# Performance work log

Hardware: AMD Instinct MI355X
Metric: run time of the kernel (lower is better)

The kernel has to match this reference:

```python
import jax, jax.numpy as jnp
import numpy as np

D_MODEL = 1024
N_HEADS = 16
HDIM = D_MODEL // N_HEADS
IMP_EPS = 1e-6


def setup_inputs() -> dict:
    key = jax.random.key(0)
    ks = jax.random.split(key, 7)
    B, T_q, T_kv, N_s = 2, 2048, 256, 16
    scale = 1.0 / np.sqrt(D_MODEL)
    return {
        "query": jax.random.normal(ks[0], (B, T_q, D_MODEL), dtype=jnp.float32),
        "key_value": jax.random.normal(ks[1], (B, T_kv, N_s, D_MODEL), dtype=jnp.float32),
        "imp_weights": jax.random.uniform(ks[2], (B, N_s), dtype=jnp.float32),
        "W_q": jax.random.normal(ks[3], (D_MODEL, D_MODEL), dtype=jnp.float32) * scale,
        "W_k": jax.random.normal(ks[4], (D_MODEL, D_MODEL), dtype=jnp.float32) * scale,
        "W_v": jax.random.normal(ks[5], (D_MODEL, D_MODEL), dtype=jnp.float32) * scale,
        "W_o": jax.random.normal(ks[6], (D_MODEL, D_MODEL), dtype=jnp.float32) * scale,
    }


def _split_heads(x):
    # [B, T, D] -> [B, h, T, d]
    B, T, _ = x.shape
    return x.reshape(B, T, N_HEADS, HDIM).transpose(0, 2, 1, 3)


def reference(query, key_value, imp_weights, W_q, W_k, W_v, W_o):
    # CAU_MultiheadCrossAttention.forward with 4D key_value (sensor axis).
    B, T_q, D = query.shape
    _, T_kv, N_s, _ = key_value.shape
    kv = key_value.reshape(B, T_kv * N_s, D)  # flatten sensor axis into source length S

    qh = _split_heads(query @ W_q.T)   # [B,h,T_q,d]  (nn.Linear: x @ W.T)
    kh = _split_heads(kv @ W_k.T)      # [B,h,S,d]
    vh = _split_heads(kv @ W_v.T)      # [B,h,S,d]

    # importance: [B,N_s] -> tiled over T_kv -> [B, S], log-clamped additive mask
    imp_full = jnp.broadcast_to(imp_weights[:, None, :], (B, T_kv, N_s)).reshape(B, T_kv * N_s)
    log_imp = jnp.log(jnp.clip(imp_full, IMP_EPS, None)).astype(qh.dtype)  # [B,S]

    scores = jnp.einsum("bhqd,bhkd->bhqk", qh, kh) / np.sqrt(HDIM).astype(np.float32)
    scores = scores + log_imp[:, None, None, :]
    attn = jax.nn.softmax(scores, axis=-1)
    y = jnp.einsum("bhqk,bhkd->bhqd", attn, vh)  # [B,h,T_q,d]

    y = y.transpose(0, 2, 1, 3).reshape(B, T_q, D)  # merge heads
    return y @ W_o.T
```

## Files before the change

kernel.cpp:

```cpp
#include <hip/hip_runtime.h>
#include <hip/hip_bf16.h>

typedef __bf16    bf16x8_t __attribute__((ext_vector_type(8)));
typedef __bf16    bf16x4_t __attribute__((ext_vector_type(4)));
typedef float     f32x4_t  __attribute__((ext_vector_type(4)));
typedef float     f32x16_t __attribute__((ext_vector_type(16)));
typedef _Float16  f16x8_t  __attribute__((ext_vector_type(8)));
typedef unsigned int u32x2_t __attribute__((ext_vector_type(2)));
typedef unsigned int u32x4_t __attribute__((ext_vector_type(4)));

static __device__ __forceinline__ f32x4_t mfma16(bf16x8_t a, bf16x8_t b, f32x4_t c) {
    return __builtin_amdgcn_mfma_f32_16x16x32_bf16(a, b, c, 0, 0, 0);
}
static __device__ __forceinline__ f32x16_t mfma32(bf16x8_t a, bf16x8_t b, f32x16_t c) {
    return __builtin_amdgcn_mfma_f32_32x32x16_bf16(a, b, c, 0, 0, 0);
}
static __device__ __forceinline__ f32x16_t zero16() {
    f32x16_t z;
#pragma unroll
    for (int j = 0; j < 16; j++) z[j] = 0.f;
    return z;
}

static __device__ __forceinline__ void async16(const __bf16* g, __bf16* l) {
    __builtin_amdgcn_global_load_lds(
        (const __attribute__((address_space(1))) unsigned int*)g,
        (__attribute__((address_space(3))) unsigned int*)l, 16, 0, 0);
}

__global__ __launch_bounds__(256) void f2b_multi(const float* __restrict__ q,
                                                 const float* __restrict__ kv,
                                                 const float* __restrict__ wq,
                                                 const float* __restrict__ wk,
                                                 const float* __restrict__ wv,
                                                 const float* __restrict__ wo,
                                                 __bf16* __restrict__ qb,
                                                 __bf16* __restrict__ kvb,
                                                 __bf16* __restrict__ wqb,
                                                 __bf16* __restrict__ wkvb,
                                                 __bf16* __restrict__ wob,
                                                 float qscale) {
    int i = blockIdx.x * 256 + threadIdx.x;
    const float* src; __bf16* dst; int base; float scale = 1.0f;
    if (i < 1048576)      { src = q;  dst = qb;   base = 0; }
    else if (i < 3145728) { src = kv; dst = kvb;  base = 1048576; }
    else if (i < 3407872) { src = wq; dst = wqb;  base = 3145728; scale = qscale; }
    else if (i < 3670016) { src = wk; dst = wkvb; base = 3407872; }
    else if (i < 3932160) { src = wv; dst = wkvb + 1048576; base = 3670016; }
    else                  { src = wo; dst = wob;  base = 3932160; }
    int j = i - base;
    float4 v = reinterpret_cast<const float4*>(src)[j];
    bf16x4_t o;
    o[0] = (__bf16)(v.x * scale); o[1] = (__bf16)(v.y * scale);
    o[2] = (__bf16)(v.z * scale); o[3] = (__bf16)(v.w * scale);
    reinterpret_cast<bf16x4_t*>(dst)[j] = o;
}

__global__ __launch_bounds__(256) void proj_kernel(const __bf16* __restrict__ qb,
                                                   const __bf16* __restrict__ wqb,
                                                   const __bf16* __restrict__ kvb,
                                                   const __bf16* __restrict__ wkvb,
                                                   __bf16* __restrict__ Qp,
                                                   __bf16* __restrict__ Khd,
                                                   __bf16* __restrict__ Vhd,
                                                   const float* __restrict__ imp) {
    __shared__ __bf16 As[128 * 32];
    __shared__ __bf16 Bs[128 * 32];
    __shared__ __bf16 Es[2][4096];

    const int gid = blockIdx.x;
    const __bf16 *A, *B;
    long m0, n0;
    int mode;
    if (gid < 256) {
        m0 = (long)(gid >> 3) * 128; n0 = (long)(gid & 7) * 128;
        A = qb; B = wqb; mode = 0;
    } else {
        int g2 = gid - 256;
        m0 = (long)(g2 >> 4) * 128; n0 = (long)(g2 & 15) * 128;
        A = kvb; B = wkvb; mode = (n0 < 1024) ? 1 : 2;
    }

    const int t    = threadIdx.x;
    const int w    = t >> 6;
    const int lane = t & 63;
    const int quad = lane >> 4;
    const int mn   = lane & 15;
    const int wm   = (w & 1) * 64;
    const int wn   = (w >> 1) * 64;

    const int  srow = t >> 2;
    const int  scol = (t & 3) * 8;
    const __bf16* gA = A + (m0 + srow) * 1024 + scol;
    const __bf16* gB = B + (n0 + srow) * 1024 + scol;

    f32x4_t acc[4][4];
#pragma unroll
    for (int i = 0; i < 4; i++)
#pragma unroll
        for (int j = 0; j < 4; j++) acc[i][j] = (f32x4_t){0.f, 0.f, 0.f, 0.f};

    for (int k0 = 0; k0 < 1024; k0 += 32) {
        __syncthreads();
        async16(gA + k0,              &As[t * 8]);
        async16(gA + 64 * 1024 + k0,  &As[2048 + t * 8]);
        async16(gB + k0,              &Bs[t * 8]);
        async16(gB + 64 * 1024 + k0,  &Bs[2048 + t * 8]);
        __syncthreads();

        bf16x8_t af[4], bf[4];
#pragma unroll
        for (int i = 0; i < 4; i++)
            af[i] = *(const bf16x8_t*)&As[(wm + i * 16 + mn) * 32 + quad * 8];
#pragma unroll
        for (int j = 0; j < 4; j++)
            bf[j] = *(const bf16x8_t*)&Bs[(wn + j * 16 + mn) * 32 + quad * 8];
#pragma unroll
        for (int i = 0; i < 4; i++)
#pragma unroll
            for (int j = 0; j < 4; j++) acc[i][j] = mfma16(af[i], bf[j], acc[i][j]);
    }

    __syncthreads();
    __bf16* stg = (w == 0) ? As : (w == 1) ? Bs : Es[w - 2];

    if (mode != 2) {
#pragma unroll
        for (int i = 0; i < 4; i++)
#pragma unroll
            for (int j = 0; j < 4; j++)
#pragma unroll
                for (int r = 0; r < 4; r++) {
                    int sl = i * 16 + quad * 4 + r;
                    int d  = j * 16 + mn;
                    stg[sl * 64 + (((d >> 3) ^ (sl & 7)) * 8) + (d & 7)] =
                        (__bf16)acc[i][j][r];
                }
    } else {
        const int b_ = (int)((m0 + wm) >> 12);
        float scl[4];
#pragma unroll
        for (int r = 0; r < 4; r++)
            scl[r] = fmaxf(imp[b_ * 16 + quad * 4 + r], 1e-6f);
#pragma unroll
        for (int i = 0; i < 4; i++)
#pragma unroll
            for (int j = 0; j < 4; j++) {
                bf16x4_t pk;
#pragma unroll
                for (int r = 0; r < 4; r++) pk[r] = (__bf16)(acc[i][j][r] * scl[r]);
                int d  = j * 16 + mn;
                int s0 = i * 16 + quad * 4;
                *(bf16x4_t*)&stg[d * 64 + (((s0 >> 3) ^ (d & 7)) * 8) + (s0 & 7)] = pk;
            }
    }

    if (mode == 0) {
        __bf16* Cg = Qp + (m0 + wm) * 1024 + (n0 + wn);
#pragma unroll
        for (int it = 0; it < 8; it++) {
            int rowL = it * 8 + (lane >> 3);
            int cb   = lane & 7;
            bf16x8_t vv = *(const bf16x8_t*)&stg[rowL * 64 + ((cb ^ (rowL & 7)) * 8)];
            *(bf16x8_t*)&Cg[(long)rowL * 1024 + cb * 8] = vv;
        }
    } else {
        const int b_    = (int)((m0 + wm) >> 12);
        const int sbase = (int)((m0 + wm) & 4095);
        __bf16* dst;
        if (mode == 1) {
            int h_ = (int)((n0 + wn) >> 6);
            dst = Khd + (long)(b_ * 16 + h_) * 262144 + (long)sbase * 64;
        } else {
            int h_ = (int)((n0 + wn) >> 6) - 16;
            dst = Vhd + (long)(b_ * 16 + h_) * 262144 + (long)(sbase >> 6) * 4096;
        }
#pragma unroll
        for (int it = 0; it < 8; it++) {
            int rowL = it * 8 + (lane >> 3);
            int cb   = lane & 7;
            bf16x8_t vv = *(const bf16x8_t*)&stg[rowL * 64 + ((cb ^ (rowL & 7)) * 8)];
            *(bf16x8_t*)&dst[rowL * 64 + cb * 8] = vv;
        }
    }
}

__global__ __launch_bounds__(256, 4) void attn_kernel(const __bf16* __restrict__ Qp,
                                                      const __bf16* __restrict__ Kh,
                                                      const __bf16* __restrict__ Vh,
                                                      const float* __restrict__ imp,
                                                      _Float16* __restrict__ Op,
                                                      float* __restrict__ Lp) {
    const int gid = blockIdx.x;
    const int qt  = (gid >> 3) & 15;
    const int sp  = (gid >> 7) & 1;
    const int bh  = ((gid >> 8) << 3) | (gid & 7);
    const int b   = bh >> 4;
    const int h   = bh & 15;
    const int t    = threadIdx.x;
    const int w    = t >> 6;
    const int lane = t & 63;
    const int hi   = lane >> 5;
    const int q32  = lane & 31;

    __shared__ __bf16 Ks[2][64 * 64];
    __shared__ __bf16 Vs[64 * 64];

    const long qrow0 = (long)b * 2048 + qt * 128 + w * 32;
    const __bf16* Kb = Kh + (long)bh * 262144;
    const __bf16* Vb = Vh + (long)bh * 262144;

    const int r8 = lane >> 3;
    const int cs = (lane & 7) ^ r8;
    const int soff    = r8 * 64 + cs * 8;
    const int srcoff0 = (0 * 4 + w) * 512 + soff;
    const int srcoff1 = (1 * 4 + w) * 512 + soff;

    bf16x8_t aq[4];
#pragma unroll
    for (int ks = 0; ks < 4; ks++)
        aq[ks] = *(const bf16x8_t*)&Qp[(qrow0 + q32) * 1024 + h * 64 + ks * 16 + hi * 8];

    float lp[2][4];
#pragma unroll
    for (int j = 0; j < 2; j++)
#pragma unroll
        for (int r = 0; r < 4; r++) lp[j][r] = 0.f;
    f32x16_t o0 = zero16(), o1 = zero16();

    const int st0 = sp * 32;

    async16(Kb + (long)st0 * 4096 + srcoff0, &Ks[0][(0 * 4 + w) * 512]);
    async16(Kb + (long)st0 * 4096 + srcoff1, &Ks[0][(1 * 4 + w) * 512]);

    const int sw8 = q32 & 7;

    for (int it = 0; it < 32; ++it) {
        const int st  = st0 + it;
        const int cur = it & 1;

        __syncthreads();

        async16(Vb + (long)st * 4096 + srcoff0, &Vs[(0 * 4 + w) * 512]);
        async16(Vb + (long)st * 4096 + srcoff1, &Vs[(1 * 4 + w) * 512]);

        const __bf16* Kc = &Ks[cur][0];
        bf16x8_t pa[4];

#pragma unroll
        for (int st2 = 0; st2 < 2; st2++) {
            f32x16_t sc = zero16();
            __builtin_amdgcn_s_setprio(1);
#pragma unroll
            for (int ks = 0; ks < 4; ks++) {
                bf16x8_t kf = *(const bf16x8_t*)
                    &Kc[(st2 * 32 + q32) * 64 + ((((ks << 1) | hi) ^ sw8) << 3)];
                sc = mfma32(kf, aq[ks], sc);
            }
            __builtin_amdgcn_s_setprio(0);

            unsigned int wv[8];
#pragma unroll
            for (int g = 0; g < 4; g++) {
                float p0 = __builtin_amdgcn_exp2f(sc[4 * g + 0]);
                float p1 = __builtin_amdgcn_exp2f(sc[4 * g + 1]);
                float p2 = __builtin_amdgcn_exp2f(sc[4 * g + 2]);
                float p3 = __builtin_amdgcn_exp2f(sc[4 * g + 3]);
                lp[g & 1][0] += p0; lp[g & 1][1] += p1;
                lp[g & 1][2] += p2; lp[g & 1][3] += p3;
                bf16x4_t pk;
                pk[0] = (__bf16)p0; pk[1] = (__bf16)p1;
                pk[2] = (__bf16)p2; pk[3] = (__bf16)p3;
                u32x2_t uu = __builtin_bit_cast(u32x2_t, pk);
                wv[2 * g]     = uu[0];
                wv[2 * g + 1] = uu[1];
            }
            u32x2_t s02 = __builtin_amdgcn_permlane32_swap(wv[0], wv[2], false, false);
            u32x2_t s13 = __builtin_amdgcn_permlane32_swap(wv[1], wv[3], false, false);
            u32x2_t s46 = __builtin_amdgcn_permlane32_swap(wv[4], wv[6], false, false);
            u32x2_t s57 = __builtin_amdgcn_permlane32_swap(wv[5], wv[7], false, false);
            u32x4_t pu0 = {s02[0], s13[0], s02[1], s13[1]};
            u32x4_t pu1 = {s46[0], s57[0], s46[1], s57[1]};
            pa[st2 * 2 + 0] = __builtin_bit_cast(bf16x8_t, pu0);
            pa[st2 * 2 + 1] = __builtin_bit_cast(bf16x8_t, pu1);
        }

        __syncthreads();

        async16(Kb + (long)(st + 1) * 4096 + srcoff0, &Ks[cur ^ 1][(0 * 4 + w) * 512]);
        async16(Kb + (long)(st + 1) * 4096 + srcoff1, &Ks[cur ^ 1][(1 * 4 + w) * 512]);

        __builtin_amdgcn_s_setprio(1);
#pragma unroll
        for (int ks = 0; ks < 4; ks++) {
            bf16x8_t v0 = *(const bf16x8_t*)
                &Vs[(0 * 32 + q32) * 64 + ((((ks << 1) | hi) ^ sw8) << 3)];
            bf16x8_t v1 = *(const bf16x8_t*)
                &Vs[(1 * 32 + q32) * 64 + ((((ks << 1) | hi) ^ sw8) << 3)];
            o0 = mfma32(pa[ks], v0, o0);
            o1 = mfma32(pa[ks], v1, o1);
        }
        __builtin_amdgcn_s_setprio(0);
    }

    float lsum = 0.f;
#pragma unroll
    for (int j = 0; j < 2; j++)
#pragma unroll
        for (int r = 0; r < 4; r++)
            lsum += lp[j][r] * fmaxf(imp[b * 16 + 4 * hi + 8 * j + r], 1e-6f);
    lsum += __shfl_xor(lsum, 32);
    if (lane < 32)
        Lp[((long)sp * 4096 + qrow0 + q32) * 16 + h] = lsum;

#pragma unroll
    for (int j = 0; j < 16; j++) {
        int q_loc = (j & 3) + 8 * (j >> 2) + 4 * hi;
        long row  = (long)sp * 4096 + qrow0 + q_loc;
        Op[row * 1024 + h * 64 + 0 * 32 + q32] = (_Float16)o0[j];
        Op[row * 1024 + h * 64 + 1 * 32 + q32] = (_Float16)o1[j];
    }
}

__global__ __launch_bounds__(256) void combine_kernel(const _Float16* __restrict__ Op,
                                                      const float* __restrict__ Lp,
                                                      __bf16* __restrict__ Y) {
    int tid = blockIdx.x * 256 + threadIdx.x;
    int row = tid >> 7;
    int cg  = tid & 127;
    int h   = cg >> 3;
    f16x8_t o0 = *(const f16x8_t*)&Op[(long)row * 1024 + cg * 8];
    f16x8_t o1 = *(const f16x8_t*)&Op[(long)(4096 + row) * 1024 + cg * 8];
    float inv = 1.0f / (Lp[row * 16 + h] + Lp[(4096 + row) * 16 + h]);
    bf16x8_t y;
#pragma unroll
    for (int j = 0; j < 8; j++) y[j] = (__bf16)(((float)o0[j] + (float)o1[j]) * inv);
    *(bf16x8_t*)&Y[(long)row * 1024 + cg * 8] = y;
}

__global__ __launch_bounds__(256) void gemm_out_kernel(const __bf16* __restrict__ A,
                                                       const __bf16* __restrict__ B,
                                                       float* __restrict__ P) {
    __shared__ __bf16 As[128 * 32];
    __shared__ __bf16 Bs[128 * 32];

    const int  kh = blockIdx.x >> 3;
    const long n0 = (long)(blockIdx.x & 7) * 128;
    const long m0 = (long)blockIdx.y * 128;
    const int  kb = kh * 512;
    float* C = P + (long)kh * 4194304;

    const int t    = threadIdx.x;
    const int w    = t >> 6;
    const int lane = t & 63;
    const int quad = lane >> 4;
    const int mn   = lane & 15;
    const int wm   = (w & 1) * 64;
    const int wn   = (w >> 1) * 64;

    const int  srow = t >> 2;
    const int  scol = (t & 3) * 8;
    const __bf16* gA = A + (m0 + srow) * 1024 + kb + scol;
    const __bf16* gB = B + (n0 + srow) * 1024 + kb + scol;

    f32x4_t acc[4][4];
#pragma unroll
    for (int i = 0; i < 4; i++)
#pragma unroll
        for (int j = 0; j < 4; j++) acc[i][j] = (f32x4_t){0.f, 0.f, 0.f, 0.f};

    for (int k0 = 0; k0 < 512; k0 += 32) {
        __syncthreads();
        async16(gA + k0,             &As[t * 8]);
        async16(gA + 64 * 1024 + k0, &As[2048 + t * 8]);
        async16(gB + k0,             &Bs[t * 8]);
        async16(gB + 64 * 1024 + k0, &Bs[2048 + t * 8]);
        __syncthreads();

        bf16x8_t af[4], bf[4];
#pragma unroll
        for (int i = 0; i < 4; i++)
            af[i] = *(const bf16x8_t*)&As[(wm + i * 16 + mn) * 32 + quad * 8];
#pragma unroll
        for (int j = 0; j < 4; j++)
            bf[j] = *(const bf16x8_t*)&Bs[(wn + j * 16 + mn) * 32 + quad * 8];
#pragma unroll
        for (int i = 0; i < 4; i++)
#pragma unroll
            for (int j = 0; j < 4; j++) acc[i][j] = mfma16(af[i], bf[j], acc[i][j]);
    }

#pragma unroll
    for (int i = 0; i < 4; i++)
#pragma unroll
        for (int j = 0; j < 4; j++)
#pragma unroll
            for (int r = 0; r < 4; r++) {
                long row = m0 + wm + i * 16 + quad * 4 + r;
                long col = n0 + wn + j * 16 + mn;
                C[row * 1024 + col] = acc[i][j][r];
            }
}

__global__ __launch_bounds__(256) void combine2_kernel(const float* __restrict__ P0,
                                                       const float* __restrict__ P1,
                                                       float* __restrict__ out) {
    int i = blockIdx.x * 256 + threadIdx.x;
    float4 a = reinterpret_cast<const float4*>(P0)[i];
    float4 b = reinterpret_cast<const float4*>(P1)[i];
    float4 c; c.x = a.x + b.x; c.y = a.y + b.y; c.z = a.z + b.z; c.w = a.w + b.w;
    reinterpret_cast<float4*>(out)[i] = c;
}

extern "C" void kernel_launch(void* const* d_in, const int* in_sizes, int n_in,
                              void* d_out, int out_size, void* d_ws, size_t ws_size,
                              hipStream_t stream) {
    const float* q_f  = (const float*)d_in[0];
    const float* kv_f = (const float*)d_in[1];
    const float* imp  = (const float*)d_in[2];
    const float* wq_f = (const float*)d_in[3];
    const float* wk_f = (const float*)d_in[4];
    const float* wv_f = (const float*)d_in[5];
    const float* wo_f = (const float*)d_in[6];

    char* ws = (char*)d_ws;
    const size_t MB = 1ull << 20;
    __bf16*   qb    = (__bf16*)(ws + 0);
    __bf16*   kvb   = (__bf16*)(ws + 8 * MB);
    __bf16*   wqb   = (__bf16*)(ws + 24 * MB);
    __bf16*   wkvb  = (__bf16*)(ws + 26 * MB);
    _Float16* Opart = (_Float16*)(ws + 0);
    float*    Lpart = (float*)(ws + 16 * MB);
    __bf16*   Yb    = (__bf16*)(ws + 17 * MB);
    __bf16*   wob   = (__bf16*)(ws + 30 * MB);
    __bf16*   Qp    = (__bf16*)(ws + 32 * MB);
    __bf16*   Khd   = (__bf16*)(ws + 40 * MB);
    __bf16*   Vhd   = (__bf16*)(ws + 56 * MB);
    float*    Gp    = (float*)(ws + 40 * MB);

    const float QSCALE = 0.125f * 1.4426950408889634f;

    f2b_multi<<<16384, 256, 0, stream>>>(q_f, kv_f, wq_f, wk_f, wv_f, wo_f,
                                         qb, kvb, wqb, wkvb, wob, QSCALE);

    proj_kernel<<<1280, 256, 0, stream>>>(qb, wqb, kvb, wkvb, Qp, Khd, Vhd, imp);

    attn_kernel<<<1024, 256, 0, stream>>>(Qp, Khd, Vhd, imp, Opart, Lpart);
    combine_kernel<<<2048, 256, 0, stream>>>(Opart, Lpart, Yb);

    gemm_out_kernel<<<dim3(16, 32), 256, 0, stream>>>(Yb, wob, Gp);
    combine2_kernel<<<4096, 256, 0, stream>>>(Gp, Gp + 4194304, (float*)d_out);
}
```

Baseline: 292.1 us.

## Store K/V tiles in fragment-major layout to drop LDS swizzle addressing

The projection epilogue now writes K and V head tiles in the order the MFMA fragments consume them (8-element chunks grouped by k-slice), not row-major with an XOR swizzle. The attention kernel then copies contiguous 16-byte chunks straight into LDS and reads each fragment at a simple lane-linear offset with constant strides. This removes the per-load XOR index arithmetic, and the contiguous per-lane reads should avoid bank conflicts. The epilogue's global writes change pattern, and the producer and consumer layouts must agree exactly.

After: 288.8 us. About the same (-1.1%).

```diff
diff --git a/kernel.cpp b/kernel.cpp
--- a/kernel.cpp
+++ b/kernel.cpp
@@ -177,10 +177,8 @@
         }
 #pragma unroll
         for (int it = 0; it < 8; it++) {
-            int rowL = it * 8 + (lane >> 3);
-            int cb   = lane & 7;
-            bf16x8_t vv = *(const bf16x8_t*)&stg[rowL * 64 + ((cb ^ (rowL & 7)) * 8)];
-            *(bf16x8_t*)&dst[rowL * 64 + cb * 8] = vv;
+            bf16x8_t vv = *(const bf16x8_t*)&stg[lane * 64 + ((it ^ (lane & 7)) * 8)];
+            *(bf16x8_t*)&dst[it * 512 + lane * 8] = vv;
         }
     }
 }
@@ -203,18 +201,15 @@
     const int hi   = lane >> 5;
     const int q32  = lane & 31;
 
-    __shared__ __bf16 Ks[2][64 * 64];
-    __shared__ __bf16 Vs[64 * 64];
+    __shared__ __bf16 Ks[2][4096];
+    __shared__ __bf16 Vs[4096];
 
     const long qrow0 = (long)b * 2048 + qt * 128 + w * 32;
     const __bf16* Kb = Kh + (long)bh * 262144;
     const __bf16* Vb = Vh + (long)bh * 262144;
 
-    const int r8 = lane >> 3;
-    const int cs = (lane & 7) ^ r8;
-    const int soff    = r8 * 64 + cs * 8;
-    const int srcoff0 = (0 * 4 + w) * 512 + soff;
-    const int srcoff1 = (1 * 4 + w) * 512 + soff;
+    const int off0 = w * 512 + lane * 8;
+    const int off1 = 2048 + w * 512 + lane * 8;
 
     bf16x8_t aq[4];
 #pragma unroll
@@ -230,10 +225,10 @@
 
     const int st0 = sp * 32;
 
-    async16(Kb + (long)st0 * 4096 + srcoff0, &Ks[0][(0 * 4 + w) * 512]);
-    async16(Kb + (long)st0 * 4096 + srcoff1, &Ks[0][(1 * 4 + w) * 512]);
-
-    const int sw8 = q32 & 7;
+    async16(Kb + (long)st0 * 4096 + off0, &Ks[0][off0]);
+    async16(Kb + (long)st0 * 4096 + off1, &Ks[0][off1]);
+
+    const int lanebase = hi * 512 + q32 * 8;
 
     for (int it = 0; it < 32; ++it) {
         const int st  = st0 + it;
@@ -241,10 +236,10 @@
 
         __syncthreads();
 
-        async16(Vb + (long)st * 4096 + srcoff0, &Vs[(0 * 4 + w) * 512]);
-        async16(Vb + (long)st * 4096 + srcoff1, &Vs[(1 * 4 + w) * 512]);
-
-        const __bf16* Kc = &Ks[cur][0];
+        async16(Vb + (long)st * 4096 + off0, &Vs[off0]);
+        async16(Vb + (long)st * 4096 + off1, &Vs[off1]);
+
+        const __bf16* Kc = &Ks[cur][lanebase];
         bf16x8_t pa[4];
 
 #pragma unroll
@@ -253,8 +248,7 @@
             __builtin_amdgcn_s_setprio(1);
 #pragma unroll
             for (int ks = 0; ks < 4; ks++) {
-                bf16x8_t kf = *(const bf16x8_t*)
-                    &Kc[(st2 * 32 + q32) * 64 + ((((ks << 1) | hi) ^ sw8) << 3)];
+                bf16x8_t kf = *(const bf16x8_t*)&Kc[ks * 1024 + st2 * 256];
                 sc = mfma32(kf, aq[ks], sc);
             }
             __builtin_amdgcn_s_setprio(0);
@@ -287,16 +281,15 @@
 
         __syncthreads();
 
-        async16(Kb + (long)(st + 1) * 4096 + srcoff0, &Ks[cur ^ 1][(0 * 4 + w) * 512]);
-        async16(Kb + (long)(st + 1) * 4096 + srcoff1, &Ks[cur ^ 1][(1 * 4 + w) * 512]);
-
+        async16(Kb + (long)(st + 1) * 4096 + off0, &Ks[cur ^ 1][off0]);
+        async16(Kb + (long)(st + 1) * 4096 + off1, &Ks[cur ^ 1][off1]);
+
+        const __bf16* Vc = &Vs[lanebase];
         __builtin_amdgcn_s_setprio(1);
 #pragma unroll
         for (int ks = 0; ks < 4; ks++) {
-            bf16x8_t v0 = *(const bf16x8_t*)
-                &Vs[(0 * 32 + q32) * 64 + ((((ks << 1) | hi) ^ sw8) << 3)];
-            bf16x8_t v1 = *(const bf16x8_t*)
-                &Vs[(1 * 32 + q32) * 64 + ((((ks << 1) | hi) ^ sw8) << 3)];
+            bf16x8_t v0 = *(const bf16x8_t*)&Vc[ks * 1024];
+            bf16x8_t v1 = *(const bf16x8_t*)&Vc[ks * 1024 + 256];
             o0 = mfma32(pa[ks], v0, o0);
             o1 = mfma32(pa[ks], v1, o1);
         }
```
